# Kernel tuning notes

Measured on AMD Instinct MI355X. Metric: run time of the kernel, lower is better.

The kernel has to match this reference:

```python
import jax, jax.numpy as jnp
import numpy as np

N_NODES = 50000
N_EDGES = 800000
N_ATOMS = 100
HID = 128
N_LAYERS = 3
OUT_LAYERS = 2
OUT_DIM = 1
N_GRAPHS = 1024
EPS = 1e-12  # F.normalize eps


def setup_inputs() -> dict:
    key = jax.random.key(0)
    ks = jax.random.split(key, 12)
    s = 0.05
    x_ori = jax.random.randint(ks[0], (N_NODES,), 0, N_ATOMS)
    edge_index = jax.random.randint(ks[1], (2, N_EDGES), 0, N_NODES)
    edge_attr = jax.random.normal(ks[2], (N_EDGES, 1), jnp.float32)
    batch_ids = jnp.sort(jax.random.randint(ks[3], (N_NODES,), 0, N_GRAPHS))
    embd_w = jax.random.normal(ks[4], (N_ATOMS, HID), jnp.float32) * s
    gamma_w = jnp.ones((N_LAYERS, N_ATOMS, 1), jnp.float32)  # reset_parameters sets ones
    w_atom_W = jax.random.normal(ks[5], (N_LAYERS, HID, HID), jnp.float32) * s
    w_atom_b = jax.random.normal(ks[6], (N_LAYERS, HID), jnp.float32) * s
    lin_W = jax.random.normal(ks[7], (OUT_LAYERS, HID, HID), jnp.float32) * s
    lin_b = jax.random.normal(ks[8], (OUT_LAYERS, HID), jnp.float32) * s
    wp_W = jax.random.normal(ks[9], (HID, OUT_DIM), jnp.float32) * s
    wp_b = jax.random.normal(ks[10], (OUT_DIM,), jnp.float32) * s
    return dict(x_ori=x_ori, edge_index=edge_index, edge_attr=edge_attr,
                batch_ids=batch_ids, embd_w=embd_w, gamma_w=gamma_w,
                w_atom_W=w_atom_W, w_atom_b=w_atom_b, lin_W=lin_W, lin_b=lin_b,
                wp_W=wp_W, wp_b=wp_b)


def reference(x_ori, edge_index, edge_attr, batch_ids, embd_w, gamma_w,
              w_atom_W, w_atom_b, lin_W, lin_b, wp_W, wp_b):
    src, dst = edge_index[0], edge_index[1]
    x = embd_w[x_ori]  # [N, H]
    for l in range(N_LAYERS):
        h = jax.nn.relu(x @ w_atom_W[l] + w_atom_b[l])            # [N, H]
        gam = jax.nn.sigmoid(gamma_w[l])[x_ori][dst]              # [E, 1]
        ew = jnp.exp(-gam * edge_attr ** 2)                       # [E, 1]
        msg = ew * h[src]                                         # [E, H] gather+weight
        agg = jax.ops.segment_sum(msg, dst, num_segments=N_NODES) # scatter-add
        y = agg + x
        nrm = jnp.maximum(jnp.linalg.norm(y, axis=1, keepdims=True), EPS)
        x = y / nrm                                               # F.normalize(., 2, 1)
    for i in range(OUT_LAYERS):
        x = jax.nn.relu(x @ lin_W[i] + lin_b[i])
    m_x = jax.ops.segment_sum(x, batch_ids, num_segments=N_GRAPHS)  # [G, H]
    props = m_x @ wp_W + wp_b                                      # [G, 1]
    return jnp.squeeze(props, axis=1)                              # [G]
```

## Files before the change

kernel.cpp:

```cpp
#include <hip/hip_runtime.h>
#include <hip/hip_bf16.h>
#include <math.h>

typedef __hip_bfloat16 bf16;
typedef unsigned int uint;
typedef unsigned short ushort;
typedef __attribute__((ext_vector_type(8))) short short8;
typedef __attribute__((ext_vector_type(4))) float f32x4;

#define HID 128
#define NN 50000
#define NE 800000
#define NG 1024
#define NA 100
#define CAP 64

__device__ __forceinline__ uint bf16_rne_hi(float f) {
    uint u = __float_as_uint(f);
    return (u + 0x7fffu + ((u >> 16) & 1u)) & 0xffff0000u;
}
__device__ __forceinline__ uint pack_bf16x2(float lo, float hi) {
    return (bf16_rne_hi(lo) >> 16) | bf16_rne_hi(hi);
}
__device__ __forceinline__ ushort bf16_rne(float f) {
    uint u = __float_as_uint(f);
    return (ushort)((u + 0x7fffu + ((u >> 16) & 1u)) >> 16);
}
__device__ __forceinline__ float load_f(const void* p, int i, int f32) {
    return f32 ? ((const float*)p)[i]
               : __uint_as_float((uint)((const ushort*)p)[i] << 16);
}
__device__ __forceinline__ int detect_f32(const void* emb) {
    const ushort* p = (const ushort*)emb;
    int lane = threadIdx.x & 63;
    float v = __uint_as_float((uint)p[lane * 4] << 16);
    int bad0 = (!(v == v) || fabsf(v) > 1e4f || (v != 0.0f && fabsf(v) < 1e-10f));
    float w = __uint_as_float((uint)p[lane * 4 + 2] << 16);
    int bad1 = (!(w == w) || fabsf(w) > 1e4f || (w != 0.0f && fabsf(w) < 1e-10f));
    int cnt = __popcll(__ballot(bad0)) + __popcll(__ballot(bad1));
    return cnt > 16;
}

#define EMB_BLKS   ((NN * 64) / 256)
#define PACKW_BLKS (5 * 16384 / 256)
#define CVT_CNT    (300 + 384 + 256 + 128 + 1)
#define CVT_BLKS   5
#define INITC_BLKS ((NN + 255) / 256)
#define PREP_B1    EMB_BLKS
#define PREP_B2    (PREP_B1 + PACKW_BLKS)
#define PREP_B3    (PREP_B2 + CVT_BLKS)
#define PREP_B4    (PREP_B3 + INITC_BLKS)
#define PREP_B5    (PREP_B4 + 4)
#define PREP_GRID  (PREP_B5 + 1)

__global__ void prep_k(const int* __restrict__ xo, const void* __restrict__ emb,
                       const void* __restrict__ gamw, const void* __restrict__ wAW,
                       const void* __restrict__ wAb, const void* __restrict__ linW,
                       const void* __restrict__ linb, const void* __restrict__ wpW,
                       const void* __restrict__ wpb,
                       uint* __restrict__ xb, ushort* __restrict__ Wp,
                       float* __restrict__ f_sgam, float* __restrict__ f_wAb,
                       float* __restrict__ f_linb, float* __restrict__ f_wp,
                       float* __restrict__ f_wpb, int* __restrict__ cursor,
                       float* __restrict__ grf, int* __restrict__ flag) {
    int f32 = detect_f32(emb);
    int b = blockIdx.x, t = threadIdx.x;
    if (b < PREP_B1) {
        int g = b * 256 + t;
        int node = g >> 6, c2 = g & 63;
        int base = xo[node] * HID + c2 * 2;
        xb[g] = pack_bf16x2(load_f(emb, base, f32), load_f(emb, base + 1, f32));
    } else if (b < PREP_B2) {
        int t2 = (b - PREP_B1) * 256 + t;
        int i   = t2 & 7;
        int n   = (t2 >> 3) & 15;
        int q   = (t2 >> 7) & 3;
        int j16 = (t2 >> 9) & 7;
        int ks  = (t2 >> 12) & 3;
        int mat = t2 >> 14;
        int k = ks * 32 + q * 8 + i;
        int j = j16 * 16 + n;
        const void* W = (mat < 3) ? wAW : linW;
        int off = ((mat < 3) ? mat : (mat - 3)) * 16384 + k * HID + j;
        Wp[t2] = bf16_rne(load_f(W, off, f32));
    } else if (b < PREP_B3) {
        int idx = (b - PREP_B2) * 256 + t;
        if (idx < 300) {
            float v = load_f(gamw, idx, f32);
            f_sgam[idx] = 1.0f / (1.0f + __expf(-v));
        } else if (idx < 684) {
            f_wAb[idx - 300] = load_f(wAb, idx - 300, f32);
        } else if (idx < 940) {
            f_linb[idx - 684] = load_f(linb, idx - 684, f32);
        } else if (idx < 1068) {
            f_wp[idx - 940] = load_f(wpW, idx - 940, f32);
        } else if (idx < CVT_CNT) {
            f_wpb[0] = load_f(wpb, 0, f32);
        }
    } else if (b < PREP_B4) {
        int n = (b - PREP_B3) * 256 + t;
        if (n < NN) cursor[n] = n * CAP;
    } else if (b < PREP_B5) {
        grf[(b - PREP_B4) * 256 + t] = 0.0f;
    } else {
        if (t == 0) *flag = f32;
    }
}

__device__ __forceinline__ void gemm_core(const uint* __restrict__ xb,
                                          const ushort* __restrict__ Wp,
                                          const float* __restrict__ bias,
                                          int m0, int lane,
                                          f32x4 acc0[8], f32x4 acc1[8]) {
    int ln15 = lane & 15;
    int q    = lane >> 4;
    int mA = min(m0 + ln15, NN - 1);
    int mB = min(m0 + 16 + ln15, NN - 1);
    const short8* A8 = (const short8*)xb;
    const short8* B8 = (const short8*)Wp;
#pragma unroll
    for (int j16 = 0; j16 < 8; ++j16) {
        float bv = bias[j16 * 16 + ln15];
        acc0[j16] = (f32x4){bv, bv, bv, bv};
        acc1[j16] = acc0[j16];
    }
#pragma unroll
    for (int ks = 0; ks < 4; ++ks) {
        short8 a0 = A8[mA * 16 + ks * 4 + q];
        short8 a1 = A8[mB * 16 + ks * 4 + q];
#pragma unroll
        for (int j16 = 0; j16 < 8; ++j16) {
            short8 b = B8[(ks * 8 + j16) * 64 + q * 16 + ln15];
            acc0[j16] = __builtin_amdgcn_mfma_f32_16x16x32_bf16(a0, b, acc0[j16], 0, 0, 0);
            acc1[j16] = __builtin_amdgcn_mfma_f32_16x16x32_bf16(a1, b, acc1[j16], 0, 0, 0);
        }
    }
}

__device__ __forceinline__ void gemm_store(f32x4 acc0[8], f32x4 acc1[8],
                                           int m0, int lane, uint* __restrict__ outb) {
    int ln15 = lane & 15;
    int q    = lane >> 4;
    ushort* ob = (ushort*)outb;
#pragma unroll
    for (int reg = 0; reg < 4; ++reg) {
        int n0 = m0 + q * 4 + reg;
        int n1 = n0 + 16;
#pragma unroll
        for (int j16 = 0; j16 < 8; ++j16) {
            if (n0 < NN)
                ob[(size_t)n0 * HID + j16 * 16 + ln15] = bf16_rne(fmaxf(acc0[j16][reg], 0.0f));
            if (n1 < NN)
                ob[(size_t)n1 * HID + j16 * 16 + ln15] = bf16_rne(fmaxf(acc1[j16][reg], 0.0f));
        }
    }
}

#define GEMM_BLKS ((NN + 127) / 128)
__global__ __launch_bounds__(256) void gemm_mfma_k(const uint* __restrict__ xb,
                                                   const ushort* __restrict__ Wp,
                                                   const float* __restrict__ bias,
                                                   uint* __restrict__ outb) {
    f32x4 acc0[8], acc1[8];
    int m0 = blockIdx.x * 128 + (threadIdx.x >> 6) * 32;
    gemm_core(xb, Wp, bias, m0, threadIdx.x & 63, acc0, acc1);
    gemm_store(acc0, acc1, m0, threadIdx.x & 63, outb);
}

#define SCAT_BLKS (NE / 4 / 256)
__global__ __launch_bounds__(256) void work2_k(const uint* __restrict__ xb,
                                               const ushort* __restrict__ Wp,
                                               const float* __restrict__ bias,
                                               uint* __restrict__ outb,
                                               const int* __restrict__ esrc,
                                               const int* __restrict__ edst,
                                               const void* __restrict__ ea,
                                               const void* __restrict__ emb,
                                               int* __restrict__ cursor,
                                               uint* __restrict__ csr) {
    int b = blockIdx.x;
    if (b < GEMM_BLKS) {
        f32x4 acc0[8], acc1[8];
        int m0 = b * 128 + (threadIdx.x >> 6) * 32;
        gemm_core(xb, Wp, bias, m0, threadIdx.x & 63, acc0, acc1);
        gemm_store(acc0, acc1, m0, threadIdx.x & 63, outb);
    } else {
        int f32 = detect_f32(emb);
        int e0 = ((b - GEMM_BLKS) * 256 + threadIdx.x) * 4;
        int4 s4 = *(const int4*)(esrc + e0);
        int4 d4 = *(const int4*)(edst + e0);
        float a0, a1, a2, a3;
        if (f32) {
            float4 f = *(const float4*)((const float*)ea + e0);
            a0 = f.x; a1 = f.y; a2 = f.z; a3 = f.w;
        } else {
            ushort4 u = *(const ushort4*)((const ushort*)ea + e0);
            a0 = __uint_as_float((uint)u.x << 16);
            a1 = __uint_as_float((uint)u.y << 16);
            a2 = __uint_as_float((uint)u.z << 16);
            a3 = __uint_as_float((uint)u.w << 16);
        }
        int p0 = atomicAdd(&cursor[d4.x], 1);
        int p1 = atomicAdd(&cursor[d4.y], 1);
        int p2 = atomicAdd(&cursor[d4.z], 1);
        int p3 = atomicAdd(&cursor[d4.w], 1);
        if (p0 < d4.x * CAP + CAP) csr[p0] = (uint)(s4.x & 0xffff) | bf16_rne_hi(a0 * a0);
        if (p1 < d4.y * CAP + CAP) csr[p1] = (uint)(s4.y & 0xffff) | bf16_rne_hi(a1 * a1);
        if (p2 < d4.z * CAP + CAP) csr[p2] = (uint)(s4.z & 0xffff) | bf16_rne_hi(a2 * a2);
        if (p3 < d4.w * CAP + CAP) csr[p3] = (uint)(s4.w & 0xffff) | bf16_rne_hi(a3 * a3);
    }
}

__global__ __launch_bounds__(256) void gemm5_graph_k(const uint* __restrict__ xb,
                                                     const ushort* __restrict__ Wp,
                                                     const float* __restrict__ bias,
                                                     const float* __restrict__ wp,
                                                     const int* __restrict__ batch,
                                                     float* __restrict__ grf) {
    int lane = threadIdx.x & 63;
    int ln15 = lane & 15;
    int q    = lane >> 4;
    int m0 = blockIdx.x * 128 + (threadIdx.x >> 6) * 32;
    f32x4 acc0[8], acc1[8];
    gemm_core(xb, Wp, bias, m0, lane, acc0, acc1);
    float wpv[8];
#pragma unroll
    for (int j16 = 0; j16 < 8; ++j16) wpv[j16] = wp[j16 * 16 + ln15];
#pragma unroll
    for (int half = 0; half < 2; ++half) {
#pragma unroll
        for (int reg = 0; reg < 4; ++reg) {
            float s = 0.0f;
#pragma unroll
            for (int j16 = 0; j16 < 8; ++j16) {
                float v = half ? acc1[j16][reg] : acc0[j16][reg];
                s = fmaf(fmaxf(v, 0.0f), wpv[j16], s);
            }
#pragma unroll
            for (int m = 1; m < 16; m <<= 1) s += __shfl_xor(s, m);
            int n = m0 + half * 16 + q * 4 + reg;
            if (ln15 == 0 && n < NN) atomicAdd(&grf[batch[n]], s);
        }
    }
}

__global__ void out_k(const float* __restrict__ grf, const float* __restrict__ wpb,
                      void* __restrict__ out, const int* __restrict__ flag) {
    int g = blockIdx.x * 256 + threadIdx.x;
    if (g >= NG) return;
    float r = grf[g] + wpb[0];
    if (*flag) ((float*)out)[g] = r;
    else       ((bf16*)out)[g] = __float2bfloat16(r);
}

__global__ void gather_norm_k(const int* __restrict__ cursor, const uint* __restrict__ csr,
                              const int* __restrict__ xo, const float* __restrict__ sgam,
                              const uint* __restrict__ hb, uint* __restrict__ xb) {
    int n = blockIdx.x * 4 + (threadIdx.x >> 6);
    int lane = threadIdx.x & 63;
    int base = n * CAP;
    int deg = min(cursor[n] - base, CAP);
    const uint* cp = csr + base;
    float g = sgam[xo[n]];
    float ax = 0.0f, ay = 0.0f;
    for (int e = 0; e < deg; e += 8) {
        uint4 c0 = *(const uint4*)(cp + e);
        uint4 c1 = *(const uint4*)(cp + e + 4);
        uint cc[8];
        cc[0] = c0.x; cc[1] = c0.y; cc[2] = c0.z; cc[3] = c0.w;
        cc[4] = c1.x; cc[5] = c1.y; cc[6] = c1.z; cc[7] = c1.w;
#pragma unroll
        for (int i = 1; i < 8; ++i) cc[i] = (e + i < deg) ? cc[i] : cc[0];
        uint v[8];
#pragma unroll
        for (int i = 0; i < 8; ++i) v[i] = hb[(cc[i] & 0xffffu) * 64 + lane];
        float w[8];
#pragma unroll
        for (int i = 0; i < 8; ++i) {
            float we = __expf(-g * __uint_as_float(cc[i] & 0xffff0000u));
            w[i] = (e + i < deg) ? we : 0.0f;
        }
#pragma unroll
        for (int i = 0; i < 8; ++i) {
            ax = fmaf(w[i], __uint_as_float(v[i] << 16), ax);
            ay = fmaf(w[i], __uint_as_float(v[i] & 0xffff0000u), ay);
        }
    }
    uint xv = xb[n * 64 + lane];
    float yx = ax + __uint_as_float(xv << 16);
    float yy = ay + __uint_as_float(xv & 0xffff0000u);
    float ss = yx * yx + yy * yy;
#pragma unroll
    for (int m = 32; m; m >>= 1) ss += __shfl_xor(ss, m);
    float inv = 1.0f / fmaxf(sqrtf(ss), 1e-12f);
    xb[n * 64 + lane] = pack_bf16x2(yx * inv, yy * inv);
}

extern "C" void kernel_launch(void* const* d_in, const int* in_sizes, int n_in,
                              void* d_out, int out_size, void* d_ws, size_t ws_size,
                              hipStream_t stream) {
    const int*  xo    = (const int*)d_in[0];
    const int*  ei    = (const int*)d_in[1];
    const int*  src   = ei;
    const int*  dst   = ei + NE;
    const void* ea    = d_in[2];
    const int*  batch = (const int*)d_in[3];
    const void* emb   = d_in[4];
    const void* gamw  = d_in[5];
    const void* wAW   = d_in[6];
    const void* wAb   = d_in[7];
    const void* linW  = d_in[8];
    const void* linb  = d_in[9];
    const void* wpW   = d_in[10];
    const void* wpb   = d_in[11];

    uint*  xb     = (uint*)d_ws;
    uint*  hb     = xb + (size_t)NN * 64;
    uint*  csr    = hb + (size_t)NN * 64;
    int*   cursor = (int*)(csr + (size_t)NN * CAP);
    float* grf    = (float*)(cursor + NN);
    float* P      = grf + NG;
    float* f_sgam = P;
    float* f_wAb  = f_sgam + 304;
    float* f_linb = f_wAb + 384;
    float* f_wp   = f_linb + 256;
    float* f_wpb  = f_wp + 128;
    int*   flag   = (int*)(f_wpb + 8);
    ushort* Wp    = (ushort*)(flag + 8);

    prep_k<<<PREP_GRID, 256, 0, stream>>>(xo, emb, gamw, wAW, wAb, linW, linb, wpW, wpb,
                                          xb, Wp, f_sgam, f_wAb, f_linb, f_wp, f_wpb,
                                          cursor, grf, flag);

    work2_k<<<GEMM_BLKS + SCAT_BLKS, 256, 0, stream>>>(xb, Wp, f_wAb, hb,
                                                       src, dst, ea, emb, cursor, csr);
    gather_norm_k<<<NN / 4, 256, 0, stream>>>(cursor, csr, xo, f_sgam, hb, xb);

    for (int l = 1; l < 3; ++l) {
        gemm_mfma_k<<<GEMM_BLKS, 256, 0, stream>>>(xb, Wp + l * 16384, f_wAb + l * HID, hb);
        gather_norm_k<<<NN / 4, 256, 0, stream>>>(cursor, csr, xo, f_sgam + l * NA,
                                                  hb, xb);
    }

    gemm_mfma_k<<<GEMM_BLKS, 256, 0, stream>>>(xb, Wp + 3 * 16384, f_linb, hb);
    gemm5_graph_k<<<GEMM_BLKS, 256, 0, stream>>>(hb, Wp + 4 * 16384, f_linb + HID,
                                                 f_wp, batch, grf);
    out_k<<<(NG + 255) / 256, 256, 0, stream>>>(grf, f_wpb, d_out, flag);
}
```

Measured before the change: 310.9 us.

## Fuse gather-normalize with next-layer GEMM via LDS staging and ping-pong h buffers

Merges each layer's edge gather, residual add and L2 normalize with the next layer's 128x128 MFMA GEMM in one kernel. Each 512-thread block builds 32 normalized rows in LDS and multiplies them by the weight matrix. The rows therefore no longer make a global round trip, and three kernel launches are dropped. Two h buffers are alternated so the gather input and the GEMM output do not alias. The trade-off is that each block reloads the full weight tile for only 32 rows and does less GEMM work per block, which may lower MFMA efficiency.

```diff
diff --git a/kernel.cpp b/kernel.cpp
--- a/kernel.cpp
+++ b/kernel.cpp
@@ -157,16 +157,6 @@
 }
 
 #define GEMM_BLKS ((NN + 127) / 128)
-__global__ __launch_bounds__(256) void gemm_mfma_k(const uint* __restrict__ xb,
-                                                   const ushort* __restrict__ Wp,
-                                                   const float* __restrict__ bias,
-                                                   uint* __restrict__ outb) {
-    f32x4 acc0[8], acc1[8];
-    int m0 = blockIdx.x * 128 + (threadIdx.x >> 6) * 32;
-    gemm_core(xb, Wp, bias, m0, threadIdx.x & 63, acc0, acc1);
-    gemm_store(acc0, acc1, m0, threadIdx.x & 63, outb);
-}
-
 #define SCAT_BLKS (NE / 4 / 256)
 __global__ __launch_bounds__(256) void work2_k(const uint* __restrict__ xb,
                                                const ushort* __restrict__ Wp,
@@ -211,6 +201,98 @@
     }
 }
 
+__global__ __launch_bounds__(512) void gg_k(const int* __restrict__ cursor,
+                                            const uint* __restrict__ csr,
+                                            const int* __restrict__ xo,
+                                            const float* __restrict__ sgam,
+                                            const uint* __restrict__ hb_in,
+                                            uint* __restrict__ xb,
+                                            const ushort* __restrict__ Wp,
+                                            const float* __restrict__ bias,
+                                            uint* __restrict__ hb_out) {
+    __shared__ uint lds_a[2048];
+    int t = threadIdx.x;
+    int w = t >> 6, lane = t & 63;
+    int n0 = blockIdx.x * 32;
+
+#pragma unroll
+    for (int j4 = 0; j4 < 4; ++j4) {
+        int j = w * 4 + j4;
+        int n = n0 + j;
+        if (n < NN) {
+            int deg = min(cursor[n] - n * CAP, CAP);
+            const uint* cp = csr + n * CAP;
+            float g = sgam[xo[n]];
+            float ax = 0.0f, ay = 0.0f;
+            for (int e = 0; e < deg; e += 8) {
+                uint4 c0 = *(const uint4*)(cp + e);
+                uint4 c1 = *(const uint4*)(cp + e + 4);
+                uint cc[8];
+                cc[0] = c0.x; cc[1] = c0.y; cc[2] = c0.z; cc[3] = c0.w;
+                cc[4] = c1.x; cc[5] = c1.y; cc[6] = c1.z; cc[7] = c1.w;
+#pragma unroll
+                for (int i = 1; i < 8; ++i) cc[i] = (e + i < deg) ? cc[i] : cc[0];
+                uint v[8];
+#pragma unroll
+                for (int i = 0; i < 8; ++i) v[i] = hb_in[(cc[i] & 0xffffu) * 64 + lane];
+                float we[8];
+#pragma unroll
+                for (int i = 0; i < 8; ++i) {
+                    float x = __expf(-g * __uint_as_float(cc[i] & 0xffff0000u));
+                    we[i] = (e + i < deg) ? x : 0.0f;
+                }
+#pragma unroll
+                for (int i = 0; i < 8; ++i) {
+                    ax = fmaf(we[i], __uint_as_float(v[i] << 16), ax);
+                    ay = fmaf(we[i], __uint_as_float(v[i] & 0xffff0000u), ay);
+                }
+            }
+            uint xv = xb[n * 64 + lane];
+            float yx = ax + __uint_as_float(xv << 16);
+            float yy = ay + __uint_as_float(xv & 0xffff0000u);
+            float ss = yx * yx + yy * yy;
+#pragma unroll
+            for (int m = 32; m; m >>= 1) ss += __shfl_xor(ss, m);
+            float inv = 1.0f / fmaxf(sqrtf(ss), 1e-12f);
+            uint o = pack_bf16x2(yx * inv, yy * inv);
+            xb[n * 64 + lane] = o;
+            int rt = j >> 4, m = j & 15;
+            int ks = lane >> 4, q = (lane >> 2) & 3;
+            lds_a[(((rt * 4 + ks) * 64) + q * 16 + m) * 4 + (lane & 3)] = o;
+        }
+    }
+    __syncthreads();
+
+    int ln15 = lane & 15, q = lane >> 4;
+    const short8* A8 = (const short8*)lds_a;
+    const short8* B8 = (const short8*)Wp;
+    f32x4 acc[2];
+    {
+        float bv = bias[w * 16 + ln15];
+        acc[0] = (f32x4){bv, bv, bv, bv};
+        acc[1] = acc[0];
+    }
+#pragma unroll
+    for (int ks = 0; ks < 4; ++ks) {
+        short8 b = B8[(ks * 8 + w) * 64 + q * 16 + ln15];
+#pragma unroll
+        for (int rt = 0; rt < 2; ++rt) {
+            short8 a = A8[(rt * 4 + ks) * 64 + lane];
+            acc[rt] = __builtin_amdgcn_mfma_f32_16x16x32_bf16(a, b, acc[rt], 0, 0, 0);
+        }
+    }
+    ushort* ob = (ushort*)hb_out;
+#pragma unroll
+    for (int rt = 0; rt < 2; ++rt) {
+#pragma unroll
+        for (int reg = 0; reg < 4; ++reg) {
+            int n = n0 + rt * 16 + q * 4 + reg;
+            if (n < NN)
+                ob[(size_t)n * HID + w * 16 + ln15] = bf16_rne(fmaxf(acc[rt][reg], 0.0f));
+        }
+    }
+}
+
 __global__ __launch_bounds__(256) void gemm5_graph_k(const uint* __restrict__ xb,
                                                      const ushort* __restrict__ Wp,
                                                      const float* __restrict__ bias,
@@ -251,49 +333,6 @@
     float r = grf[g] + wpb[0];
     if (*flag) ((float*)out)[g] = r;
     else       ((bf16*)out)[g] = __float2bfloat16(r);
-}
-
-__global__ void gather_norm_k(const int* __restrict__ cursor, const uint* __restrict__ csr,
-                              const int* __restrict__ xo, const float* __restrict__ sgam,
-                              const uint* __restrict__ hb, uint* __restrict__ xb) {
-    int n = blockIdx.x * 4 + (threadIdx.x >> 6);
-    int lane = threadIdx.x & 63;
-    int base = n * CAP;
-    int deg = min(cursor[n] - base, CAP);
-    const uint* cp = csr + base;
-    float g = sgam[xo[n]];
-    float ax = 0.0f, ay = 0.0f;
-    for (int e = 0; e < deg; e += 8) {
-        uint4 c0 = *(const uint4*)(cp + e);
-        uint4 c1 = *(const uint4*)(cp + e + 4);
-        uint cc[8];
-        cc[0] = c0.x; cc[1] = c0.y; cc[2] = c0.z; cc[3] = c0.w;
-        cc[4] = c1.x; cc[5] = c1.y; cc[6] = c1.z; cc[7] = c1.w;
-#pragma unroll
-        for (int i = 1; i < 8; ++i) cc[i] = (e + i < deg) ? cc[i] : cc[0];
-        uint v[8];
-#pragma unroll
-        for (int i = 0; i < 8; ++i) v[i] = hb[(cc[i] & 0xffffu) * 64 + lane];
-        float w[8];
-#pragma unroll
-        for (int i = 0; i < 8; ++i) {
-            float we = __expf(-g * __uint_as_float(cc[i] & 0xffff0000u));
-            w[i] = (e + i < deg) ? we : 0.0f;
-        }
-#pragma unroll
-        for (int i = 0; i < 8; ++i) {
-            ax = fmaf(w[i], __uint_as_float(v[i] << 16), ax);
-            ay = fmaf(w[i], __uint_as_float(v[i] & 0xffff0000u), ay);
-        }
-    }
-    uint xv = xb[n * 64 + lane];
-    float yx = ax + __uint_as_float(xv << 16);
-    float yy = ay + __uint_as_float(xv & 0xffff0000u);
-    float ss = yx * yx + yy * yy;
-#pragma unroll
-    for (int m = 32; m; m >>= 1) ss += __shfl_xor(ss, m);
-    float inv = 1.0f / fmaxf(sqrtf(ss), 1e-12f);
-    xb[n * 64 + lane] = pack_bf16x2(yx * inv, yy * inv);
 }
 
 extern "C" void kernel_launch(void* const* d_in, const int* in_sizes, int n_in,
@@ -315,8 +354,9 @@
     const void* wpb   = d_in[11];
 
     uint*  xb     = (uint*)d_ws;
-    uint*  hb     = xb + (size_t)NN * 64;
-    uint*  csr    = hb + (size_t)NN * 64;
+    uint*  hA     = xb + (size_t)NN * 64;
+    uint*  hB     = hA + (size_t)NN * 64;
+    uint*  csr    = hB + (size_t)NN * 64;
     int*   cursor = (int*)(csr + (size_t)NN * CAP);
     float* grf    = (float*)(cursor + NN);
     float* P      = grf + NG;
@@ -332,18 +372,18 @@
                                           xb, Wp, f_sgam, f_wAb, f_linb, f_wp, f_wpb,
                                           cursor, grf, flag);
 
-    work2_k<<<GEMM_BLKS + SCAT_BLKS, 256, 0, stream>>>(xb, Wp, f_wAb, hb,
+    work2_k<<<GEMM_BLKS + SCAT_BLKS, 256, 0, stream>>>(xb, Wp, f_wAb, hA,
                                                        src, dst, ea, emb, cursor, csr);
-    gather_norm_k<<<NN / 4, 256, 0, stream>>>(cursor, csr, xo, f_sgam, hb, xb);
-
-    for (int l = 1; l < 3; ++l) {
-        gemm_mfma_k<<<GEMM_BLKS, 256, 0, stream>>>(xb, Wp + l * 16384, f_wAb + l * HID, hb);
-        gather_norm_k<<<NN / 4, 256, 0, stream>>>(cursor, csr, xo, f_sgam + l * NA,
-                                                  hb, xb);
-    }
-
-    gemm_mfma_k<<<GEMM_BLKS, 256, 0, stream>>>(xb, Wp + 3 * 16384, f_linb, hb);
-    gemm5_graph_k<<<GEMM_BLKS, 256, 0, stream>>>(hb, Wp + 4 * 16384, f_linb + HID,
+
+    const int GG_GRID = (NN + 31) / 32;
+    gg_k<<<GG_GRID, 512, 0, stream>>>(cursor, csr, xo, f_sgam,       hA, xb,
+                                      Wp + 1 * 16384, f_wAb + 128, hB);
+    gg_k<<<GG_GRID, 512, 0, stream>>>(cursor, csr, xo, f_sgam + 100, hB, xb,
+                                      Wp + 2 * 16384, f_wAb + 256, hA);
+    gg_k<<<GG_GRID, 512, 0, stream>>>(cursor, csr, xo, f_sgam + 200, hA, xb,
+                                      Wp + 3 * 16384, f_linb,       hB);
+
+    gemm5_graph_k<<<GEMM_BLKS, 256, 0, stream>>>(hB, Wp + 4 * 16384, f_linb + HID,
                                                  f_wp, batch, grf);
     out_k<<<(NG + 255) / 256, 256, 0, stream>>>(grf, f_wpb, d_out, flag);
 }
```

Measured after the change: 296.5 us. -4.6%, faster.
